# Kernel tuning notes

Hardware: AMD Instinct MI355X
Metric: run time of the kernel (lower is better)

## Reference

```python
import jax, jax.numpy as jnp
import numpy as np

C = 16          # number of classes (label values in [0, C))
K = 2048        # int(args.d * args.overlap_ratio) = int(4096 * 0.5)
ALPHA = 1.0     # args.alpha margin
EPS = 1e-6      # nn.PairwiseDistance eps (added elementwise to the diff)


def setup_inputs() -> dict:
    key = jax.random.key(0)
    k1, k2 = jax.random.split(key)
    x = jax.random.normal(k1, (65536, 256), dtype=jnp.float32)
    y = jax.random.randint(k2, (65536, 3), 0, C, dtype=jnp.int64)
    return {"x": x, "y": y}


def reference(x, y):
    labels = y[:, 2]                                   # [N]
    member = labels[None, :] == jnp.arange(C)[:, None]  # [C, N] bool class membership
    counts = member.sum(axis=1).astype(x.dtype)         # [C]

    # per-class centers (mean of member rows)
    centers = (member.astype(x.dtype) @ x) / counts[:, None]  # [C, D]

    # PairwiseDistance(p=2, eps): ||center - x + eps||_2. Since eps is added
    # elementwise to the diff, this equals the distance between (center+eps) and x,
    # so the standard ||a||^2 - 2a.b + ||b||^2 expansion applies with shifted centers.
    c = centers + EPS                                   # [C, D]
    d2 = ((c * c).sum(axis=1)[:, None]                  # [C, 1]
          - 2.0 * (c @ x.T)                             # [C, N]
          + (x * x).sum(axis=1)[None, :])               # [1, N]
    D = jnp.sqrt(jnp.maximum(d2, 0.0))                  # [C, N]

    inf = jnp.asarray(jnp.inf, dtype=x.dtype)

    # positives: for class c, K LARGEST distances from center_c to class-c points
    pos_masked = jnp.where(member, D, -inf)             # [C, N]
    pos_k = jax.lax.top_k(pos_masked, K)[0]             # [C, K]
    pos_mean = pos_k.mean(axis=1)                       # [C]
    pos_var = pos_k.var(axis=1, ddof=1)                 # [C] (torch .var is unbiased)
    pos_stat = pos_mean + 1.96 * jnp.sqrt(pos_var)      # [C]

    # negatives: for pair (c1, c2), K SMALLEST distances from center_c1 to class-c2 points
    neg_masked = jnp.where(member[None, :, :], D[:, None, :], inf)  # [C, C, N]
    neg_k = -jax.lax.top_k(-neg_masked, K)[0]           # [C, C, K]
    neg_mean = neg_k.mean(axis=-1)                      # [C, C]
    neg_var = neg_k.var(axis=-1, ddof=1)                # [C, C]
    neg_stat = neg_mean - 1.96 * jnp.sqrt(neg_var)      # [C, C]

    terms = jnp.maximum(ALPHA + pos_stat[:, None] - neg_stat, 0.0)  # [C, C]
    offdiag = 1.0 - jnp.eye(C, dtype=x.dtype)           # skip class_type2 == class_type1
    loss = (terms * offdiag).sum()
    return loss.reshape(1)
```

## Files before the change

### kernel.cpp

```cpp
#include <hip/hip_runtime.h>
#include <cfloat>
#include <cstdint>

#define NPTS 65536
#define DIM 256
#define NC 16
#define KSEL 2048
#define VMAX 4608
#define EPSV 1e-6f

typedef __attribute__((ext_vector_type(8))) short short8v;
typedef __attribute__((ext_vector_type(4))) float f32x4;


__global__ void __launch_bounds__(256) k_histrank(const int* __restrict__ y,
                                                  int* __restrict__ bhist,
                                                  int* __restrict__ slots) {
  __shared__ int labs[256];
  __shared__ int wcnt[4][NC];
  int t = threadIdx.x;
  int chunk = blockIdx.x;
  labs[t] = y[(chunk * 256 + t) * 3 + 2];
  __syncthreads();
  int lab = labs[t];
  int lane = t & 63, w = t >> 6;
  unsigned long long mymask = 0;
#pragma unroll
  for (int c = 0; c < NC; ++c) {
    unsigned long long mk = __ballot(lab == c);
    if (lane == 0) wcnt[w][c] = __popcll(mk);
    if (lab == c) mymask = mk;
  }
  __syncthreads();
  int rank = __popcll(mymask & ((1ull << lane) - 1ull));
  for (int w2 = 0; w2 < w; ++w2) rank += wcnt[w2][lab];
  slots[chunk * 256 + t] = (lab << 16) | rank;
  if (t < NC) bhist[chunk * NC + t] = wcnt[0][t] + wcnt[1][t] + wcnt[2][t] + wcnt[3][t];
}

__global__ void __launch_bounds__(256) k_scan(int* __restrict__ bhist,
                                              int* __restrict__ counts,
                                              int* __restrict__ offsets) {
  __shared__ int lh[256 * NC];
  __shared__ int segbase[16][NC];
  __shared__ int totl[NC], offl[NC];
  int t = threadIdx.x;
  for (int u = t; u < 256 * NC; u += 256) lh[u] = bhist[u];
  __syncthreads();
  int c = t & 15, g = t >> 4;
  int part = 0;
#pragma unroll
  for (int b = 0; b < 16; ++b) part += lh[(g * 16 + b) * NC + c];
  segbase[g][c] = part;
  __syncthreads();
  if (t < NC) {
    int tot = 0;
#pragma unroll
    for (int g2 = 0; g2 < 16; ++g2) tot += segbase[g2][t];
    totl[t] = tot;
    counts[t] = tot;
  }
  __syncthreads();
  if (t == 0) {
    int run = 0;
    for (int c2 = 0; c2 < NC; ++c2) { offl[c2] = run; offsets[c2] = run; run += totl[c2]; }
  }
  __syncthreads();
  if (t < NC) {
    int run = offl[t];
#pragma unroll
    for (int g2 = 0; g2 < 16; ++g2) { int tmp = segbase[g2][t]; segbase[g2][t] = run; run += tmp; }
  }
  __syncthreads();
  int run = segbase[g][c];
#pragma unroll
  for (int b = 0; b < 16; ++b) {
    int idx = (g * 16 + b) * NC + c;
    int tmp = lh[idx]; lh[idx] = run; run += tmp;
  }
  __syncthreads();
  for (int u = t; u < 256 * NC; u += 256) bhist[u] = lh[u];
}

#define ACC_CASE(C) case C: acc[C][0] += xv[u].x; acc[C][1] += xv[u].y; \
                            acc[C][2] += xv[u].z; acc[C][3] += xv[u].w; break;

__global__ void __launch_bounds__(256) k_accum(const float* __restrict__ x,
                                               const int* __restrict__ y,
                                               float* __restrict__ partials) {
  __shared__ int labs[128];
  __shared__ float red[2 * NC * DIM];
  int t = threadIdx.x;
  int n0 = blockIdx.x * 128;
  if (t < 128) labs[t] = y[(n0 + t) * 3 + 2];
  __syncthreads();
  int w = t >> 6, m = t & 63;

  float acc[NC][4];
#pragma unroll
  for (int c = 0; c < NC; ++c)
#pragma unroll
    for (int j = 0; j < 4; ++j) acc[c][j] = 0.f;

  for (int r0 = 0; r0 < 32; r0 += 4) {
    float4 xv[4];
#pragma unroll
    for (int u = 0; u < 4; ++u)
      xv[u] = *(const float4*)(x + (size_t)(n0 + 32 * w + r0 + u) * DIM + 4 * m);
#pragma unroll
    for (int u = 0; u < 4; ++u) {
      int lab = __builtin_amdgcn_readfirstlane(labs[32 * w + r0 + u]);
      switch (lab) {
        ACC_CASE(0) ACC_CASE(1) ACC_CASE(2) ACC_CASE(3)
        ACC_CASE(4) ACC_CASE(5) ACC_CASE(6) ACC_CASE(7)
        ACC_CASE(8) ACC_CASE(9) ACC_CASE(10) ACC_CASE(11)
        ACC_CASE(12) ACC_CASE(13) ACC_CASE(14) ACC_CASE(15)
      }
    }
  }

  int half = w & 1;
  if (w < 2) {
#pragma unroll
    for (int c = 0; c < NC; ++c)
#pragma unroll
      for (int j = 0; j < 4; ++j)
        red[half * (NC * DIM) + c * DIM + 4 * m + j] = acc[c][j];
  }
  __syncthreads();
  if (w >= 2) {
#pragma unroll
    for (int c = 0; c < NC; ++c)
#pragma unroll
      for (int j = 0; j < 4; ++j)
        red[half * (NC * DIM) + c * DIM + 4 * m + j] += acc[c][j];
  }
  __syncthreads();
  for (int u = t; u < NC * DIM; u += 256)
    partials[(size_t)blockIdx.x * (NC * DIM) + u] = red[u] + red[NC * DIM + u];
}

__global__ void __launch_bounds__(256) k_reduce(const float* __restrict__ partials,
                                                float* __restrict__ partial2) {
  int tg = blockIdx.x * 256 + threadIdx.x;
  int u = tg & 4095;
  int s = tg >> 12;
  float acc = 0.f;
#pragma unroll 8
  for (int b = s * 64; b < s * 64 + 64; ++b)
    acc += partials[(size_t)b * (NC * DIM) + u];
  partial2[s * 4096 + u] = acc;
}

__global__ void __launch_bounds__(256) k_centers(const float* __restrict__ partial2,
                                                 const int* __restrict__ gcounts,
                                                 float* __restrict__ centers,
                                                 float* __restrict__ csq,
                                                 unsigned short* __restrict__ cfb) {
  __shared__ float wsum[4];
  int d = threadIdx.x, c = blockIdx.x;
  float v = 0.f;
#pragma unroll
  for (int s = 0; s < 8; ++s) v += partial2[s * 4096 + c * DIM + d];
  v = v / (float)gcounts[c] + EPSV;
  centers[c * DIM + d] = v;
  unsigned int bits = __float_as_uint(v);
  unsigned short h = (unsigned short)((bits + 0x7FFFu + ((bits >> 16) & 1u)) >> 16);
  int kc = d >> 5, lg = (d >> 3) & 3, j = d & 7;
  int l = lg * 16 + c;
  cfb[kc * 512 + l * 8 + j] = h;
  float q = v * v;
#pragma unroll
  for (int m = 1; m < 64; m <<= 1) q += __shfl_xor(q, m);
  if ((d & 63) == 0) wsum[d >> 6] = q;
  __syncthreads();
  if (d == 0) csq[c] = wsum[0] + wsum[1] + wsum[2] + wsum[3];
}

__device__ __forceinline__ unsigned int cvt_pk_bf16(float lo, float hi) {
  unsigned int r;
  asm("v_cvt_pk_bf16_f32 %0, %1, %2" : "=v"(r) : "v"(lo), "v"(hi));
  return r;
}

__global__ void __launch_bounds__(256) k_dist(const float* __restrict__ x,
                                              const unsigned short* __restrict__ cfb,
                                              const float* __restrict__ csq,
                                              const int* __restrict__ slots,
                                              const int* __restrict__ bbase,
                                              float* __restrict__ Dmat) {
  __shared__ float csql[NC];
  __shared__ int baseL[NC];
  __shared__ int slotL[64];
  int t = threadIdx.x;
  if (t < NC) {
    csql[t] = csq[t];
    baseL[t] = bbase[(blockIdx.x >> 2) * NC + t];
  }
  __syncthreads();
  int pbase = blockIdx.x * 64;
  if (t < 64) {
    int sp = slots[pbase + t];
    slotL[t] = baseL[sp >> 16] + (sp & 0xFFFF);
  }
  __syncthreads();

  int wave = t >> 6, l = t & 63;
  int lg = l >> 4;
  int pl = wave * 16 + (l & 15);
  int p = pbase + pl;

  const float4* xrow = (const float4*)(x + (size_t)p * DIM);
  float4 xa[8][2];
#pragma unroll
  for (int kc = 0; kc < 8; ++kc) {
    xa[kc][0] = xrow[kc * 8 + lg * 2 + 0];
    xa[kc][1] = xrow[kc * 8 + lg * 2 + 1];
  }

  float xsq = 0.f;
#pragma unroll
  for (int kc = 0; kc < 8; ++kc) {
    float4 a0 = xa[kc][0], a1 = xa[kc][1];
    xsq += a0.x * a0.x + a0.y * a0.y + a0.z * a0.z + a0.w * a0.w +
           a1.x * a1.x + a1.y * a1.y + a1.z * a1.z + a1.w * a1.w;
  }
  xsq += __shfl_xor(xsq, 16);
  xsq += __shfl_xor(xsq, 32);

  const uint4* cfp = (const uint4*)cfb;
  f32x4 acc = {0.f, 0.f, 0.f, 0.f};
#pragma unroll
  for (int kc = 0; kc < 8; ++kc) {
    union { unsigned int u[4]; short8v s; } xb, cf;
    float4 a0 = xa[kc][0], a1 = xa[kc][1];
    xb.u[0] = cvt_pk_bf16(a0.x, a0.y);
    xb.u[1] = cvt_pk_bf16(a0.z, a0.w);
    xb.u[2] = cvt_pk_bf16(a1.x, a1.y);
    xb.u[3] = cvt_pk_bf16(a1.z, a1.w);
    uint4 cw = cfp[kc * 64 + l];
    cf.u[0] = cw.x; cf.u[1] = cw.y; cf.u[2] = cw.z; cf.u[3] = cw.w;
    acc = __builtin_amdgcn_mfma_f32_16x16x32_bf16(cf.s, xb.s, acc, 0, 0, 0);
  }

  int slot = slotL[pl];
#pragma unroll
  for (int j = 0; j < 4; ++j) {
    int m = lg * 4 + j;
    float d2 = csql[m] - 2.f * acc[j] + xsq;
    Dmat[(size_t)m * NPTS + slot] = sqrtf(fmaxf(d2, 0.f));
  }
}

__global__ void __launch_bounds__(512) k_select(const float* __restrict__ Dmat,
                                                const int* __restrict__ gcounts,
                                                const int* __restrict__ offsets,
                                                float* __restrict__ pos_stat,
                                                float* __restrict__ neg_stat) {
  __shared__ unsigned int keys[VMAX];
  __shared__ int hist[2048];
  __shared__ int bsel[2];
  __shared__ float wsumf[8];
  __shared__ int wsumi[8];
  int tid = threadIdx.x;
  int lane = tid & 63, wv = tid >> 6;
  int b = blockIdx.x;
  int ci = b >> 4, cl = b & 15;
  bool largest = (ci == cl);
  int cnt = gcounts[cl];
  if (cnt > VMAX) cnt = VMAX;
  int off = offsets[cl];
  const float* src = Dmat + (size_t)ci * NPTS + off;
  unsigned int inv = largest ? 0xFFFFFFFFu : 0u;
  for (int t = tid; t < cnt; t += 512) keys[t] = __float_as_uint(src[t]) ^ inv;
  __syncthreads();

  int target = KSEL;
  unsigned int pfx = 0;

  for (int u = tid; u < 2048; u += 512) hist[u] = 0;
  __syncthreads();
  for (int t = tid; t < cnt; t += 512) atomicAdd(&hist[keys[t] >> 21], 1);
  __syncthreads();
  if (tid < 64) {
    int own = 0;
#pragma unroll
    for (int j = 0; j < 32; ++j) own += hist[lane * 32 + j];
    int incl = own;
    for (int o = 1; o < 64; o <<= 1) { int n = __shfl_up(incl, o); if (lane >= o) incl += n; }
    int excl = incl - own;
    unsigned long long mk = __ballot(excl < target && target <= incl);
    int sel = __ffsll((unsigned long long)mk) - 1;
    if (lane == sel) {
      int run = excl;
      for (int j = 0; j < 32; ++j) {
        int h = hist[lane * 32 + j];
        if (run < target && target <= run + h) { bsel[0] = lane * 32 + j; bsel[1] = target - run; }
        run += h;
      }
    }
  }
  __syncthreads();
  pfx = ((unsigned int)bsel[0]) << 21; target = bsel[1];
  __syncthreads();

  for (int u = tid; u < 2048; u += 512) hist[u] = 0;
  __syncthreads();
  for (int t = tid; t < cnt; t += 512) {
    unsigned int k = keys[t];
    if ((k >> 21) == (pfx >> 21)) atomicAdd(&hist[(k >> 10) & 0x7FF], 1);
  }
  __syncthreads();
  if (tid < 64) {
    int own = 0;
#pragma unroll
    for (int j = 0; j < 32; ++j) own += hist[lane * 32 + j];
    int incl = own;
    for (int o = 1; o < 64; o <<= 1) { int n = __shfl_up(incl, o); if (lane >= o) incl += n; }
    int excl = incl - own;
    unsigned long long mk = __ballot(excl < target && target <= incl);
    int sel = __ffsll((unsigned long long)mk) - 1;
    if (lane == sel) {
      int run = excl;
      for (int j = 0; j < 32; ++j) {
        int h = hist[lane * 32 + j];
        if (run < target && target <= run + h) { bsel[0] = lane * 32 + j; bsel[1] = target - run; }
        run += h;
      }
    }
  }
  __syncthreads();
  pfx |= ((unsigned int)bsel[0]) << 10; target = bsel[1];
  __syncthreads();

  for (int u = tid; u < 1024; u += 512) hist[u] = 0;
  __syncthreads();
  for (int t = tid; t < cnt; t += 512) {
    unsigned int k = keys[t];
    if ((k >> 10) == (pfx >> 10)) atomicAdd(&hist[k & 0x3FF], 1);
  }
  __syncthreads();
  if (tid < 64) {
    int own = 0;
#pragma unroll
    for (int j = 0; j < 16; ++j) own += hist[lane * 16 + j];
    int incl = own;
    for (int o = 1; o < 64; o <<= 1) { int n = __shfl_up(incl, o); if (lane >= o) incl += n; }
    int excl = incl - own;
    unsigned long long mk = __ballot(excl < target && target <= incl);
    int sel = __ffsll((unsigned long long)mk) - 1;
    if (lane == sel) {
      int run = excl;
      for (int j = 0; j < 16; ++j) {
        int h = hist[lane * 16 + j];
        if (run < target && target <= run + h) { bsel[0] = lane * 16 + j; }
        run += h;
      }
    }
  }
  __syncthreads();
  unsigned int T = pfx | (unsigned int)bsel[0];
  float fT = __uint_as_float(T ^ inv);

  int nl = 0; float sl = 0.f;
  for (int t = tid; t < cnt; t += 512) {
    unsigned int k = keys[t];
    if (k < T) { nl++; sl += __uint_as_float(k ^ inv); }
  }
#pragma unroll
  for (int m = 1; m < 64; m <<= 1) { nl += __shfl_xor(nl, m); sl += __shfl_xor(sl, m); }
  if (lane == 0) { wsumi[wv] = nl; wsumf[wv] = sl; }
  __syncthreads();
  int n_less = 0; float s_less = 0.f;
#pragma unroll
  for (int w2 = 0; w2 < 8; ++w2) { n_less += wsumi[w2]; s_less += wsumf[w2]; }
  float mean = (s_less + (float)(KSEL - n_less) * fT) / (float)KSEL;
  __syncthreads();

  float sv = 0.f;
  for (int t = tid; t < cnt; t += 512) {
    unsigned int k = keys[t];
    if (k < T) { float d = __uint_as_float(k ^ inv) - mean; sv += d * d; }
  }
#pragma unroll
  for (int m = 1; m < 64; m <<= 1) sv += __shfl_xor(sv, m);
  if (lane == 0) wsumf[wv] = sv;
  __syncthreads();
  if (tid == 0) {
    float vs = 0.f;
#pragma unroll
    for (int w2 = 0; w2 < 8; ++w2) vs += wsumf[w2];
    float dT = fT - mean;
    float var = (vs + (float)(KSEL - n_less) * dT * dT) / (float)(KSEL - 1);
    if (largest) pos_stat[ci] = mean + 1.96f * sqrtf(var);
    else neg_stat[ci * 16 + cl] = mean - 1.96f * sqrtf(var);
  }
}

__global__ void __launch_bounds__(256) k_loss(const float* __restrict__ pos_stat,
                                              const float* __restrict__ neg_stat,
                                              float* __restrict__ out) {
  __shared__ float red[256];
  int t = threadIdx.x;
  int i = t >> 4, c = t & 15;
  float v = 0.f;
  if (i != c) v = fmaxf(1.0f + pos_stat[i] - neg_stat[t], 0.f);
  red[t] = v; __syncthreads();
  for (int st = 128; st > 0; st >>= 1) { if (t < st) red[t] += red[t + st]; __syncthreads(); }
  if (t == 0) out[0] = red[0];
}

extern "C" void kernel_launch(void* const* d_in, const int* in_sizes, int n_in,
                              void* d_out, int out_size, void* d_ws, size_t ws_size,
                              hipStream_t stream) {
  const float* x = (const float*)d_in[0];
  const int* y = (const int*)d_in[1];
  float* out = (float*)d_out;
  char* ws = (char*)d_ws;

  int* counts = (int*)(ws + 16384);
  int* offsets = (int*)(ws + 16512);
  float* csq = (float*)(ws + 16576);
  float* pos_stat = (float*)(ws + 16640);
  float* neg_stat = (float*)(ws + 16704);
  float* centers = (float*)(ws + 17728);
  int* bhist = (int*)(ws + 34112);
  unsigned short* cfb = (unsigned short*)(ws + 50688);
  float* Dmat = (float*)(ws + 65536);
  float* partials = (float*)(ws + 65536);
  int* slots = (int*)(ws + 16842752);
  float* partial2 = (float*)(ws + 33554432);

  k_histrank<<<256, 256, 0, stream>>>(y, bhist, slots);
  k_scan<<<1, 256, 0, stream>>>(bhist, counts, offsets);
  k_accum<<<512, 256, 0, stream>>>(x, y, partials);
  k_reduce<<<128, 256, 0, stream>>>(partials, partial2);
  k_centers<<<16, 256, 0, stream>>>(partial2, counts, centers, csq, cfb);
  k_dist<<<1024, 256, 0, stream>>>(x, cfb, csq, slots, bhist, Dmat);
  k_select<<<256, 512, 0, stream>>>(Dmat, counts, offsets, pos_stat, neg_stat);
  k_loss<<<1, 256, 0, stream>>>(pos_stat, neg_stat, out);
}
```

Before: 72.15 us.

## Fuse histogram/rank into accum and merge reduce, centers and scan kernels

The label histogram and per-block ranking move into k_accum, which now writes slots and per-128-row block histograms. k_reduce, k_centers and k_scan are merged into one 17-block launch: 16 blocks reduce partials and build the bf16 centers and squared norms, and one block does the prefix scan. This cuts the pipeline from eight launches to five and drops the partial2 round trip. In exchange, the reduction now runs on only 16 blocks of 1024 threads, which may lower parallelism for the 512-way partial sum.

Result: no change. 73.52 us (+1.9%).

```diff
diff --git a/kernel.cpp b/kernel.cpp
--- a/kernel.cpp
+++ b/kernel.cpp
@@ -13,89 +13,43 @@
 typedef __attribute__((ext_vector_type(4))) float f32x4;
 
 
-__global__ void __launch_bounds__(256) k_histrank(const int* __restrict__ y,
-                                                  int* __restrict__ bhist,
-                                                  int* __restrict__ slots) {
-  __shared__ int labs[256];
-  __shared__ int wcnt[4][NC];
-  int t = threadIdx.x;
-  int chunk = blockIdx.x;
-  labs[t] = y[(chunk * 256 + t) * 3 + 2];
-  __syncthreads();
-  int lab = labs[t];
-  int lane = t & 63, w = t >> 6;
-  unsigned long long mymask = 0;
-#pragma unroll
-  for (int c = 0; c < NC; ++c) {
-    unsigned long long mk = __ballot(lab == c);
-    if (lane == 0) wcnt[w][c] = __popcll(mk);
-    if (lab == c) mymask = mk;
-  }
-  __syncthreads();
-  int rank = __popcll(mymask & ((1ull << lane) - 1ull));
-  for (int w2 = 0; w2 < w; ++w2) rank += wcnt[w2][lab];
-  slots[chunk * 256 + t] = (lab << 16) | rank;
-  if (t < NC) bhist[chunk * NC + t] = wcnt[0][t] + wcnt[1][t] + wcnt[2][t] + wcnt[3][t];
-}
-
-__global__ void __launch_bounds__(256) k_scan(int* __restrict__ bhist,
-                                              int* __restrict__ counts,
-                                              int* __restrict__ offsets) {
-  __shared__ int lh[256 * NC];
-  __shared__ int segbase[16][NC];
-  __shared__ int totl[NC], offl[NC];
-  int t = threadIdx.x;
-  for (int u = t; u < 256 * NC; u += 256) lh[u] = bhist[u];
-  __syncthreads();
-  int c = t & 15, g = t >> 4;
-  int part = 0;
-#pragma unroll
-  for (int b = 0; b < 16; ++b) part += lh[(g * 16 + b) * NC + c];
-  segbase[g][c] = part;
-  __syncthreads();
-  if (t < NC) {
-    int tot = 0;
-#pragma unroll
-    for (int g2 = 0; g2 < 16; ++g2) tot += segbase[g2][t];
-    totl[t] = tot;
-    counts[t] = tot;
-  }
-  __syncthreads();
-  if (t == 0) {
-    int run = 0;
-    for (int c2 = 0; c2 < NC; ++c2) { offl[c2] = run; offsets[c2] = run; run += totl[c2]; }
-  }
-  __syncthreads();
-  if (t < NC) {
-    int run = offl[t];
-#pragma unroll
-    for (int g2 = 0; g2 < 16; ++g2) { int tmp = segbase[g2][t]; segbase[g2][t] = run; run += tmp; }
-  }
-  __syncthreads();
-  int run = segbase[g][c];
-#pragma unroll
-  for (int b = 0; b < 16; ++b) {
-    int idx = (g * 16 + b) * NC + c;
-    int tmp = lh[idx]; lh[idx] = run; run += tmp;
-  }
-  __syncthreads();
-  for (int u = t; u < 256 * NC; u += 256) bhist[u] = lh[u];
-}
-
 #define ACC_CASE(C) case C: acc[C][0] += xv[u].x; acc[C][1] += xv[u].y; \
                             acc[C][2] += xv[u].z; acc[C][3] += xv[u].w; break;
 
 __global__ void __launch_bounds__(256) k_accum(const float* __restrict__ x,
                                                const int* __restrict__ y,
-                                               float* __restrict__ partials) {
+                                               float* __restrict__ partials,
+                                               int* __restrict__ bhist,
+                                               int* __restrict__ slots) {
   __shared__ int labs[128];
+  __shared__ int wcnt2[2][NC];
   __shared__ float red[2 * NC * DIM];
   int t = threadIdx.x;
   int n0 = blockIdx.x * 128;
   if (t < 128) labs[t] = y[(n0 + t) * 3 + 2];
   __syncthreads();
+
+  if (t < 128) {
+    int lab = labs[t];
+    int lane = t & 63, w2 = t >> 6;
+    unsigned long long mymask = 0;
+#pragma unroll
+    for (int c = 0; c < NC; ++c) {
+      unsigned long long mk = __ballot(lab == c);
+      if (lane == 0) wcnt2[w2][c] = __popcll(mk);
+      if (lab == c) mymask = mk;
+    }
+    int rank = __popcll(mymask & ((1ull << lane) - 1ull));
+    slots[n0 + t] = (lab << 16) | rank;
+  }
+  __syncthreads();
+  if (t >= 64 && t < 128) {
+    int lab = labs[t];
+    slots[n0 + t] += wcnt2[0][lab];
+  }
+  if (t < NC) bhist[blockIdx.x * NC + t] = wcnt2[0][t] + wcnt2[1][t];
+
   int w = t >> 6, m = t & 63;
-
   float acc[NC][4];
 #pragma unroll
   for (int c = 0; c < NC; ++c)
@@ -140,41 +94,101 @@
     partials[(size_t)blockIdx.x * (NC * DIM) + u] = red[u] + red[NC * DIM + u];
 }
 
-__global__ void __launch_bounds__(256) k_reduce(const float* __restrict__ partials,
-                                                float* __restrict__ partial2) {
-  int tg = blockIdx.x * 256 + threadIdx.x;
-  int u = tg & 4095;
-  int s = tg >> 12;
-  float acc = 0.f;
+__global__ void __launch_bounds__(1024) k_redcent(const float* __restrict__ partials,
+                                                  const int* __restrict__ bhist,
+                                                  int* __restrict__ bhist2,
+                                                  int* __restrict__ counts,
+                                                  int* __restrict__ offsets,
+                                                  float* __restrict__ csq,
+                                                  unsigned short* __restrict__ cfb) {
+  __shared__ int lh[512 * NC];
+  __shared__ float sl[4 * 256];
+  __shared__ int segbase[16][NC];
+  __shared__ int totl[NC], offl[NC];
+  __shared__ int wredi[16];
+  __shared__ int cnt_sh;
+  __shared__ float wsum[4];
+  int t = threadIdx.x;
+
+  if (blockIdx.x < 16) {
+    int c = blockIdx.x;
+    int d = t & 255, s = t >> 8;
+    float a = 0.f;
 #pragma unroll 8
-  for (int b = s * 64; b < s * 64 + 64; ++b)
-    acc += partials[(size_t)b * (NC * DIM) + u];
-  partial2[s * 4096 + u] = acc;
-}
-
-__global__ void __launch_bounds__(256) k_centers(const float* __restrict__ partial2,
-                                                 const int* __restrict__ gcounts,
-                                                 float* __restrict__ centers,
-                                                 float* __restrict__ csq,
-                                                 unsigned short* __restrict__ cfb) {
-  __shared__ float wsum[4];
-  int d = threadIdx.x, c = blockIdx.x;
-  float v = 0.f;
-#pragma unroll
-  for (int s = 0; s < 8; ++s) v += partial2[s * 4096 + c * DIM + d];
-  v = v / (float)gcounts[c] + EPSV;
-  centers[c * DIM + d] = v;
-  unsigned int bits = __float_as_uint(v);
-  unsigned short h = (unsigned short)((bits + 0x7FFFu + ((bits >> 16) & 1u)) >> 16);
-  int kc = d >> 5, lg = (d >> 3) & 3, j = d & 7;
-  int l = lg * 16 + c;
-  cfb[kc * 512 + l * 8 + j] = h;
-  float q = v * v;
-#pragma unroll
-  for (int m = 1; m < 64; m <<= 1) q += __shfl_xor(q, m);
-  if ((d & 63) == 0) wsum[d >> 6] = q;
-  __syncthreads();
-  if (d == 0) csq[c] = wsum[0] + wsum[1] + wsum[2] + wsum[3];
+    for (int b = s * 128; b < s * 128 + 128; ++b)
+      a += partials[(size_t)b * (NC * DIM) + c * DIM + d];
+    sl[s * 256 + d] = a;
+
+    int lane = t & 63, wv = t >> 6;
+    int v = (t < 512) ? bhist[t * NC + c] : 0;
+#pragma unroll
+    for (int m = 1; m < 64; m <<= 1) v += __shfl_xor(v, m);
+    if (lane == 0) wredi[wv] = v;
+    __syncthreads();
+    if (t == 0) {
+      int cn = 0;
+#pragma unroll
+      for (int w2 = 0; w2 < 16; ++w2) cn += wredi[w2];
+      cnt_sh = cn;
+    }
+    __syncthreads();
+    if (s == 0) {
+      float v4 = sl[d] + sl[256 + d] + sl[512 + d] + sl[768 + d];
+      float vc = v4 / (float)cnt_sh + EPSV;
+      unsigned int bits = __float_as_uint(vc);
+      unsigned short h = (unsigned short)((bits + 0x7FFFu + ((bits >> 16) & 1u)) >> 16);
+      int kc = d >> 5, lg = (d >> 3) & 3, j = d & 7;
+      int l = lg * 16 + c;
+      cfb[kc * 512 + l * 8 + j] = h;
+      float q = vc * vc;
+#pragma unroll
+      for (int m = 1; m < 64; m <<= 1) q += __shfl_xor(q, m);
+      if ((d & 63) == 0) wsum[d >> 6] = q;
+    }
+    __syncthreads();
+    if (t == 0) csq[c] = wsum[0] + wsum[1] + wsum[2] + wsum[3];
+  } else {
+    for (int u = t; u < 512 * NC; u += 1024) lh[u] = bhist[u];
+    __syncthreads();
+    if (t < 256) {
+      int c = t & 15, g = t >> 4;
+      int part = 0;
+#pragma unroll
+      for (int b = 0; b < 32; ++b) part += lh[(g * 32 + b) * NC + c];
+      segbase[g][c] = part;
+    }
+    __syncthreads();
+    if (t < NC) {
+      int tot = 0;
+#pragma unroll
+      for (int g2 = 0; g2 < 16; ++g2) tot += segbase[g2][t];
+      totl[t] = tot;
+      counts[t] = tot;
+    }
+    __syncthreads();
+    if (t == 0) {
+      int run = 0;
+      for (int c2 = 0; c2 < NC; ++c2) { offl[c2] = run; offsets[c2] = run; run += totl[c2]; }
+    }
+    __syncthreads();
+    if (t < NC) {
+      int run = offl[t];
+#pragma unroll
+      for (int g2 = 0; g2 < 16; ++g2) { int tmp = segbase[g2][t]; segbase[g2][t] = run; run += tmp; }
+    }
+    __syncthreads();
+    if (t < 256) {
+      int c = t & 15, g = t >> 4;
+      int run = segbase[g][c];
+#pragma unroll
+      for (int b = 0; b < 32; ++b) {
+        int idx = (g * 32 + b) * NC + c;
+        int tmp = lh[idx]; lh[idx] = run; run += tmp;
+      }
+    }
+    __syncthreads();
+    for (int u = t; u < 512 * NC; u += 1024) bhist2[u] = lh[u];
+  }
 }
 
 __device__ __forceinline__ unsigned int cvt_pk_bf16(float lo, float hi) {
@@ -195,7 +209,7 @@
   int t = threadIdx.x;
   if (t < NC) {
     csql[t] = csq[t];
-    baseL[t] = bbase[(blockIdx.x >> 2) * NC + t];
+    baseL[t] = bbase[(blockIdx.x >> 1) * NC + t];
   }
   __syncthreads();
   int pbase = blockIdx.x * 64;
@@ -418,25 +432,21 @@
   float* out = (float*)d_out;
   char* ws = (char*)d_ws;
 
-  int* counts = (int*)(ws + 16384);
-  int* offsets = (int*)(ws + 16512);
-  float* csq = (float*)(ws + 16576);
-  float* pos_stat = (float*)(ws + 16640);
-  float* neg_stat = (float*)(ws + 16704);
-  float* centers = (float*)(ws + 17728);
-  int* bhist = (int*)(ws + 34112);
-  unsigned short* cfb = (unsigned short*)(ws + 50688);
-  float* Dmat = (float*)(ws + 65536);
-  float* partials = (float*)(ws + 65536);
+  int* bhist = (int*)(ws + 0);
+  int* counts = (int*)(ws + 32768);
+  int* offsets = (int*)(ws + 32832);
+  float* csq = (float*)(ws + 32896);
+  float* pos_stat = (float*)(ws + 32960);
+  float* neg_stat = (float*)(ws + 33024);
+  unsigned short* cfb = (unsigned short*)(ws + 34048);
+  int* bhist2 = (int*)(ws + 65536);
+  float* Dmat = (float*)(ws + 131072);
+  float* partials = (float*)(ws + 131072);
   int* slots = (int*)(ws + 16842752);
-  float* partial2 = (float*)(ws + 33554432);
-
-  k_histrank<<<256, 256, 0, stream>>>(y, bhist, slots);
-  k_scan<<<1, 256, 0, stream>>>(bhist, counts, offsets);
-  k_accum<<<512, 256, 0, stream>>>(x, y, partials);
-  k_reduce<<<128, 256, 0, stream>>>(partials, partial2);
-  k_centers<<<16, 256, 0, stream>>>(partial2, counts, centers, csq, cfb);
-  k_dist<<<1024, 256, 0, stream>>>(x, cfb, csq, slots, bhist, Dmat);
+
+  k_accum<<<512, 256, 0, stream>>>(x, y, partials, bhist, slots);
+  k_redcent<<<17, 1024, 0, stream>>>(partials, bhist, bhist2, counts, offsets, csq, cfb);
+  k_dist<<<1024, 256, 0, stream>>>(x, cfb, csq, slots, bhist2, Dmat);
   k_select<<<256, 512, 0, stream>>>(Dmat, counts, offsets, pos_stat, neg_stat);
   k_loss<<<1, 256, 0, stream>>>(pos_stat, neg_stat, out);
 }
```
